# Performance work log

Measured on AMD Instinct MI355X. Metric: run time of the kernel, lower is better.

Reference implementation:

```python
import jax, jax.numpy as jnp
import numpy as np
import math

D_MODEL = 256
H = 8
D_K = D_MODEL // H
POS_OFFSET = 20
GRID = 7  # module hard-codes key_padding_mask.view(bs, 7, 7)


def _sine_pos_table(num_pos_feats=D_MODEL // 2, temperature=10000, rng=(-20, 20)):
    # faithful port of position_embedding_sine with normalize=True
    scale = 2 * math.pi
    emb = np.arange(rng[0], rng[1] + 1, dtype=np.float32)
    emb = emb / (emb[-1] + 1e-6) * scale  # normalize by last element (=20)
    dim_t = np.arange(num_pos_feats, dtype=np.float32)
    dim_t = temperature ** (2.0 * np.floor(dim_t / 2.0) / num_pos_feats)
    pos = emb[:, None] / dim_t  # [41, 128]
    pos = np.stack((np.sin(pos[:, 0::2]), np.cos(pos[:, 1::2])), axis=-1).reshape(pos.shape[0], -1)
    return jnp.asarray(pos, dtype=jnp.float32)  # [41, 128]


def setup_inputs() -> dict:
    key = jax.random.key(0)
    ks = jax.random.split(key, 8)
    L, B, D = 49, 2048, D_MODEL
    query = jax.random.normal(ks[0], (L, B, D), dtype=jnp.float32)
    key_t = jax.random.normal(ks[1], (L, B, D), dtype=jnp.float32)
    value = jax.random.normal(ks[2], (L, B, D), dtype=jnp.float32)
    key_padding_mask = jnp.zeros((B, L), dtype=bool)  # no padding
    # parameters (xavier-ish init)
    lim = math.sqrt(6.0 / (3 * D + D))
    in_proj_weight = jax.random.uniform(ks[3], (3 * D, D), minval=-lim, maxval=lim, dtype=jnp.float32)
    in_proj_bias = jnp.zeros((3 * D,), dtype=jnp.float32)
    out_w = jax.random.uniform(ks[4], (D, D), minval=-1.0 / math.sqrt(D), maxval=1.0 / math.sqrt(D), dtype=jnp.float32)
    out_b = jnp.zeros((D,), dtype=jnp.float32)
    pos_x = _sine_pos_table()  # [41, 128]
    pos_y = _sine_pos_table()  # [41, 128]
    return {"query": query, "key": key_t, "value": value,
            "key_padding_mask": key_padding_mask,
            "in_proj_weight": in_proj_weight, "in_proj_bias": in_proj_bias,
            "out_w": out_w, "out_b": out_b, "pos_x": pos_x, "pos_y": pos_y}


def reference(query, key, value, key_padding_mask, in_proj_weight, in_proj_bias, out_w, out_b, pos_x, pos_y):
    L, B, D = query.shape
    S = key.shape[0]
    scaling = float(D_K) ** -0.5
    w_q, w_k, w_v = in_proj_weight[:D], in_proj_weight[D:2 * D], in_proj_weight[2 * D:]
    b_q, b_k, b_v = in_proj_bias[:D], in_proj_bias[D:2 * D], in_proj_bias[2 * D:]
    q = (query @ w_q.T + b_q) * scaling          # [L, B, D]
    k = key @ w_k.T + b_k                        # [S, B, D]
    v = value @ w_v.T + b_v                      # [S, B, D]
    # [B, H, L, d_k] etc.
    q4 = q.reshape(L, B, H, D_K).transpose(1, 2, 0, 3)
    k4 = k.reshape(S, B, H, D_K).transpose(1, 2, 0, 3)
    v4 = v.reshape(S, B, H, D_K).transpose(1, 2, 0, 3)
    attn = jnp.einsum('bhld,bhsd->bhls', q4, k4)  # [B, H, L, S]
    # relative position indices from cumsum over the 7x7 grid
    img_mask = (~key_padding_mask).reshape(B, GRID, GRID)
    yy = jnp.cumsum(img_mask.astype(jnp.float32), axis=1).reshape(B, -1)
    xx = jnp.cumsum(img_mask.astype(jnp.float32), axis=2).reshape(B, -1)
    idx_yy = (yy[:, :, None] - yy[:, None, :] + POS_OFFSET).astype(jnp.int32)  # [B, HW, HW]
    idx_xx = (xx[:, :, None] - xx[:, None, :] + POS_OFFSET).astype(jnp.int32)
    # project positional tables through the key weights (faithful slicing)
    k_posy = jnp.einsum('pf,df->pd', pos_y, w_k[:, :D // 2])  # [41, D]
    k_posx = jnp.einsum('pf,df->pd', pos_x, w_k[:, D // 2:])  # [41, D]
    P = k_posy.shape[0]
    k_posy = k_posy.reshape(P, H, D_K)
    k_posx = k_posx.reshape(P, H, D_K)
    posy = jnp.einsum('bhld,phd->bhlp', q4, k_posy)  # [B, H, HW, 41]
    posx = jnp.einsum('bhld,phd->bhlp', q4, k_posx)
    gy = jnp.take_along_axis(posy, jnp.broadcast_to(idx_yy[:, None], posy.shape[:3] + (S,)), axis=-1)
    gx = jnp.take_along_axis(posx, jnp.broadcast_to(idx_xx[:, None], posx.shape[:3] + (S,)), axis=-1)
    attn = attn + gy + gx
    attn = jnp.where(key_padding_mask[:, None, None, :], -jnp.inf, attn)
    attn = jax.nn.softmax(attn, axis=-1)  # dropout skipped (eval mode)
    out = jnp.einsum('bhls,bhsd->bhld', attn, v4)        # [B, H, L, d_k]
    out = out.transpose(2, 0, 1, 3).reshape(L, B, D)     # [L, B, D]
    out = out @ out_w.T + out_b
    return out
```

## Files before the change

kernel.cpp:

```cpp
#include <hip/hip_runtime.h>
#include <hip/hip_bf16.h>

#define L_Q 49
#define D_MODEL 256
#define NHEAD 8
#define DK 32
#define PP 41
#define POS_OFF 20

typedef __attribute__((ext_vector_type(8))) __bf16 bf16x8;
typedef __attribute__((ext_vector_type(4))) float f32x4;
typedef __attribute__((ext_vector_type(8))) unsigned short u16x8;

__device__ __forceinline__ float bf2f(unsigned short u) {
    return __uint_as_float(((unsigned)u) << 16);
}
__device__ __forceinline__ unsigned short f2bf(float f) {
    unsigned u = __float_as_uint(f);
    return (unsigned short)((u + 0x7FFF + ((u >> 16) & 1)) >> 16);
}

__global__ __launch_bounds__(256)
void convert_w(const float* __restrict__ W, const float* __restrict__ out_w,
               float scaling,
               unsigned short* __restrict__ wbf, unsigned short* __restrict__ owbf) {
    int i = blockIdx.x * 256 + threadIdx.x;
    if (i < 49152) {
        int row = i >> 6;
        float sc = (row < 256) ? scaling : 1.0f;
        float4 v = reinterpret_cast<const float4*>(W)[i];
        ushort4 o = { f2bf(v.x * sc), f2bf(v.y * sc), f2bf(v.z * sc), f2bf(v.w * sc) };
        reinterpret_cast<ushort4*>(wbf)[i] = o;
    } else {
        float4 v = reinterpret_cast<const float4*>(out_w)[i - 49152];
        ushort4 o = { f2bf(v.x), f2bf(v.y), f2bf(v.z), f2bf(v.w) };
        reinterpret_cast<ushort4*>(owbf)[i - 49152] = o;
    }
}

__global__ __launch_bounds__(256)
void prep_kpos(const float* __restrict__ pos_y, const float* __restrict__ pos_x,
               const float* __restrict__ W, unsigned short* __restrict__ kpb) {
    int p = blockIdx.x;
    int which = blockIdx.y;
    __shared__ float pr[128];
    int d = threadIdx.x;
    if (d < 128) pr[d] = which ? pos_x[p * 128 + d] : pos_y[p * 128 + d];
    __syncthreads();
    const float* Wk = W + 256 * 256;
    int fOff = which ? 128 : 0;
    float acc = 0.f;
    #pragma unroll 8
    for (int f = 0; f < 128; ++f)
        acc += pr[f] * Wk[(size_t)d * 256 + fOff + f];
    kpb[((size_t)which * PP + p) * 256 + d] = f2bf(acc);
}

__global__ __launch_bounds__(512)
void proj_mfma(const float* __restrict__ Xq, const float* __restrict__ Xk,
               const float* __restrict__ Xv,
               const unsigned short* __restrict__ Wb,
               const float* __restrict__ bias, float scaling,
               unsigned short* __restrict__ outq, unsigned short* __restrict__ outk,
               unsigned short* __restrict__ outv) {
    __shared__ unsigned short Wl[65536];
    __shared__ float Lb[256];
    int which = blockIdx.y;
    const float* X = (which == 0) ? Xq : ((which == 1) ? Xk : Xv);
    unsigned short* out = (which == 0) ? outq : ((which == 1) ? outk : outv);
    const unsigned short* wsrc = Wb + (size_t)which * 65536;

    int tid = threadIdx.x, wid = tid >> 6, lane = tid & 63;
    int rgrp = lane & 15, kgrp = lane >> 4;

    #pragma unroll
    for (int it = 0; it < 16; ++it) {
        int c = wid + it * 8;
        unsigned dst = (unsigned)c * 1024 + (unsigned)lane * 16;
        unsigned n = dst >> 9;
        unsigned gs = dst ^ ((n & 7) << 4);
        __builtin_amdgcn_global_load_lds((const char*)wsrc + gs,
                                         (char*)Wl + (size_t)c * 1024, 16, 0, 0);
    }
    if (tid < 256) Lb[tid] = bias[which * 256 + tid] * ((which == 0) ? scaling : 1.0f);

    size_t xrow = (size_t)blockIdx.x * 128 + wid * 16 + rgrp;
    const float* xp = X + xrow * 256 + kgrp * 8;
    float4 pa0 = *reinterpret_cast<const float4*>(xp);
    float4 pa1 = *reinterpret_cast<const float4*>(xp + 4);
    __syncthreads();

    f32x4 acc[16];
    #pragma unroll
    for (int i = 0; i < 16; ++i) acc[i] = (f32x4){0.f, 0.f, 0.f, 0.f};

    unsigned lbase = ((unsigned)rgrp * 512 + (unsigned)kgrp * 16) ^ ((rgrp & 7) << 4);

    #pragma unroll
    for (int kk = 0; kk < 8; ++kk) {
        float4 a0 = pa0, a1 = pa1;
        if (kk < 7) {
            pa0 = *reinterpret_cast<const float4*>(xp + (kk + 1) * 32);
            pa1 = *reinterpret_cast<const float4*>(xp + (kk + 1) * 32 + 4);
        }
        union { unsigned short s[8]; bf16x8 v; } xu;
        xu.s[0] = f2bf(a0.x); xu.s[1] = f2bf(a0.y); xu.s[2] = f2bf(a0.z); xu.s[3] = f2bf(a0.w);
        xu.s[4] = f2bf(a1.x); xu.s[5] = f2bf(a1.y); xu.s[6] = f2bf(a1.z); xu.s[7] = f2bf(a1.w);
        unsigned kb = lbase ^ (unsigned)(kk * 64);
        #pragma unroll
        for (int nt = 0; nt < 16; ++nt) {
            bf16x8 wf = *reinterpret_cast<const bf16x8*>((const char*)Wl + kb + nt * 8192);
            acc[nt] = __builtin_amdgcn_mfma_f32_16x16x32_bf16(wf, xu.v, acc[nt], 0, 0, 0);
        }
    }

    #pragma unroll
    for (int nt = 0; nt < 16; ++nt) {
        float4 bv = *reinterpret_cast<const float4*>(&Lb[nt * 16 + kgrp * 4]);
        ushort4 pk;
        pk.x = f2bf(acc[nt][0] + bv.x);
        pk.y = f2bf(acc[nt][1] + bv.y);
        pk.z = f2bf(acc[nt][2] + bv.z);
        pk.w = f2bf(acc[nt][3] + bv.w);
        *reinterpret_cast<ushort4*>(&out[xrow * 256 + nt * 16 + kgrp * 4]) = pk;
    }
}

__global__ __launch_bounds__(512)
void out_mfma(const unsigned short* __restrict__ Xb, const unsigned short* __restrict__ Wb,
              const float* __restrict__ bias, float* __restrict__ out) {
    __shared__ unsigned short Wl[65536];
    __shared__ float Lb[256];
    int tid = threadIdx.x, wid = tid >> 6, lane = tid & 63;
    int rgrp = lane & 15, kgrp = lane >> 4;

    #pragma unroll
    for (int it = 0; it < 16; ++it) {
        int c = wid + it * 8;
        unsigned dst = (unsigned)c * 1024 + (unsigned)lane * 16;
        unsigned n = dst >> 9;
        unsigned gs = dst ^ ((n & 7) << 4);
        __builtin_amdgcn_global_load_lds((const char*)Wb + gs,
                                         (char*)Wl + (size_t)c * 1024, 16, 0, 0);
    }
    if (tid < 256) Lb[tid] = bias[tid];

    size_t xrow = (size_t)blockIdx.x * 128 + wid * 16 + rgrp;
    const unsigned short* xp = Xb + xrow * 256 + kgrp * 8;
    bf16x8 pa = *reinterpret_cast<const bf16x8*>(xp);
    __syncthreads();

    f32x4 acc[16];
    #pragma unroll
    for (int i = 0; i < 16; ++i) acc[i] = (f32x4){0.f, 0.f, 0.f, 0.f};

    unsigned lbase = ((unsigned)rgrp * 512 + (unsigned)kgrp * 16) ^ ((rgrp & 7) << 4);

    #pragma unroll
    for (int kk = 0; kk < 8; ++kk) {
        bf16x8 af = pa;
        if (kk < 7) pa = *reinterpret_cast<const bf16x8*>(xp + (kk + 1) * 32);
        unsigned kb = lbase ^ (unsigned)(kk * 64);
        #pragma unroll
        for (int nt = 0; nt < 16; ++nt) {
            bf16x8 wf = *reinterpret_cast<const bf16x8*>((const char*)Wl + kb + nt * 8192);
            acc[nt] = __builtin_amdgcn_mfma_f32_16x16x32_bf16(wf, af, acc[nt], 0, 0, 0);
        }
    }

    #pragma unroll
    for (int nt = 0; nt < 16; ++nt) {
        float4 bv = *reinterpret_cast<const float4*>(&Lb[nt * 16 + kgrp * 4]);
        float4 o;
        o.x = acc[nt][0] + bv.x;
        o.y = acc[nt][1] + bv.y;
        o.z = acc[nt][2] + bv.z;
        o.w = acc[nt][3] + bv.w;
        *reinterpret_cast<float4*>(&out[xrow * 256 + nt * 16 + kgrp * 4]) = o;
    }
}

__global__ __launch_bounds__(256)
void attn_mfma(const unsigned short* __restrict__ qbuf,
               const unsigned short* __restrict__ kbuf,
               const unsigned short* __restrict__ vbuf,
               const unsigned short* __restrict__ kpb,
               const unsigned char* __restrict__ mask,
               unsigned short* __restrict__ ctx,
               int B) {
    __shared__ unsigned short Kp[96][40];
    __shared__ unsigned short Pt[64][72];
    __shared__ unsigned short Vt[32][72];
    __shared__ unsigned short postab[49][40];
    __shared__ int yy[L_Q], xx[L_Q];
    __shared__ unsigned char mb[52];

    int b = blockIdx.x, h = blockIdx.y;
    int tid = threadIdx.x, wid = tid >> 6, lane = tid & 63;
    int rgrp = lane & 15, kgrp = lane >> 4;
    size_t lstride = (size_t)B * D_MODEL;
    size_t base = (size_t)b * D_MODEL + (size_t)h * DK;

    if (tid < L_Q) mb[tid] = mask[(size_t)b * L_Q + tid];
    if (tid < 196) {
        int l = tid >> 2, c = tid & 3;
        u16x8 vv = *reinterpret_cast<const u16x8*>(vbuf + (size_t)l * lstride + base + c * 8);
        #pragma unroll
        for (int j = 0; j < 8; ++j) Vt[c * 8 + j][l] = vv[j];
    }
    for (int e = tid; e < 512; e += 256) {
        int d = e >> 4, s2 = 48 + (e & 15);
        if (s2 > 48) Vt[d][s2] = 0;
    }
    for (int t = tid; t < 384; t += 256) {
        int r = t >> 2, kc = t & 3;
        const unsigned short* src;
        if (r < 64) {
            int kr = min(r, 48);
            src = kbuf + (size_t)kr * lstride + base + kc * 8;
        } else if (r < 80) {
            int p = r - 64 + 13;
            src = kpb + (size_t)p * D_MODEL + h * DK + kc * 8;
        } else {
            int p = r - 80 + 13;
            src = kpb + (size_t)(PP + p) * D_MODEL + h * DK + kc * 8;
        }
        *reinterpret_cast<u16x8*>(&Kp[r][kc * 8]) = *reinterpret_cast<const u16x8*>(src);
    }
    __syncthreads();
    if (tid < L_Q) {
        int r = tid / 7, c = tid % 7;
        int sy = 0, sx = 0;
        for (int rr = 0; rr <= r; ++rr) sy += (mb[rr * 7 + c] == 0);
        for (int cc = 0; cc <= c; ++cc) sx += (mb[r * 7 + cc] == 0);
        yy[tid] = sy; xx[tid] = sx;
    }
    __syncthreads();

    int qrow = min(16 * wid + rgrp, 48);
    bf16x8 qfrag = *reinterpret_cast<const bf16x8*>(qbuf + (size_t)qrow * lstride + base + kgrp * 8);
    f32x4 acc[6];
    #pragma unroll
    for (int t = 0; t < 6; ++t) {
        bf16x8 bfrag = *reinterpret_cast<const bf16x8*>(&Kp[t * 16 + rgrp][kgrp * 8]);
        acc[t] = __builtin_amdgcn_mfma_f32_16x16x32_bf16(qfrag, bfrag,
                    (f32x4){0.f, 0.f, 0.f, 0.f}, 0, 0, 0);
    }

    #pragma unroll
    for (int i = 0; i < 4; ++i) {
        int l = 16 * wid + kgrp * 4 + i;
        if (l <= 48) {
            postab[l][rgrp]      = f2bf(acc[4][i]);
            postab[l][20 + rgrp] = f2bf(acc[5][i]);
        }
    }
    asm volatile("s_waitcnt lgkmcnt(0)" ::: "memory");

    #pragma unroll
    for (int i = 0; i < 4; ++i) {
        int l = 16 * wid + kgrp * 4 + i;
        int lc = min(l, 48);
        int yyl = yy[lc], xxl = xx[lc];
        float v[4];
        #pragma unroll
        for (int ct = 0; ct < 4; ++ct) {
            int s = ct * 16 + rgrp;
            int sc = min(s, 48);
            int iy = yyl - yy[sc] + (POS_OFF - 13);
            int ix = xxl - xx[sc] + (POS_OFF - 13);
            float val = acc[ct][i] + bf2f(postab[lc][iy]) + bf2f(postab[lc][20 + ix]);
            v[ct] = (s >= L_Q || mb[sc]) ? -1e30f : val;
        }
        float m = fmaxf(fmaxf(v[0], v[1]), fmaxf(v[2], v[3]));
        m = fmaxf(m, __shfl_xor(m, 1));
        m = fmaxf(m, __shfl_xor(m, 2));
        m = fmaxf(m, __shfl_xor(m, 4));
        m = fmaxf(m, __shfl_xor(m, 8));
        float ssum = 0.f, ex[4];
        #pragma unroll
        for (int ct = 0; ct < 4; ++ct) { ex[ct] = __expf(v[ct] - m); ssum += ex[ct]; }
        ssum += __shfl_xor(ssum, 1);
        ssum += __shfl_xor(ssum, 2);
        ssum += __shfl_xor(ssum, 4);
        ssum += __shfl_xor(ssum, 8);
        float is = 1.f / ssum;
        #pragma unroll
        for (int ct = 0; ct < 4; ++ct)
            Pt[l & 63][ct * 16 + rgrp] = f2bf(ex[ct] * is);
    }
    asm volatile("s_waitcnt lgkmcnt(0)" ::: "memory");

    f32x4 oacc[2];
    oacc[0] = (f32x4){0.f, 0.f, 0.f, 0.f};
    oacc[1] = (f32x4){0.f, 0.f, 0.f, 0.f};
    #pragma unroll
    for (int kc = 0; kc < 2; ++kc) {
        bf16x8 pa = *reinterpret_cast<const bf16x8*>(&Pt[16 * wid + rgrp][kc * 32 + kgrp * 8]);
        #pragma unroll
        for (int dt = 0; dt < 2; ++dt) {
            bf16x8 vb = *reinterpret_cast<const bf16x8*>(&Vt[dt * 16 + rgrp][kc * 32 + kgrp * 8]);
            oacc[dt] = __builtin_amdgcn_mfma_f32_16x16x32_bf16(pa, vb, oacc[dt], 0, 0, 0);
        }
    }
    #pragma unroll
    for (int dt = 0; dt < 2; ++dt)
        #pragma unroll
        for (int i = 0; i < 4; ++i) {
            int l = 16 * wid + kgrp * 4 + i;
            if (l <= 48)
                ctx[(size_t)l * lstride + base + dt * 16 + rgrp] = f2bf(oacc[dt][i]);
        }
}

extern "C" void kernel_launch(void* const* d_in, const int* in_sizes, int n_in,
                              void* d_out, int out_size, void* d_ws, size_t ws_size,
                              hipStream_t stream) {
    const float* query = (const float*)d_in[0];
    const float* key   = (const float*)d_in[1];
    const float* value = (const float*)d_in[2];
    const unsigned char* maskp = (const unsigned char*)d_in[3];
    const float* W     = (const float*)d_in[4];
    const float* bias  = (const float*)d_in[5];
    const float* out_w = (const float*)d_in[6];
    const float* out_b = (const float*)d_in[7];
    const float* pos_x = (const float*)d_in[8];
    const float* pos_y = (const float*)d_in[9];
    float* out = (float*)d_out;

    int B = in_sizes[0] / (L_Q * D_MODEL);
    int M = L_Q * B;

    size_t nqkv = (size_t)M * D_MODEL;
    unsigned short* qb = (unsigned short*)d_ws;
    unsigned short* kb = qb + nqkv;
    unsigned short* vb = kb + nqkv;
    unsigned short* kpb = vb + nqkv;
    unsigned short* wbf = kpb + 2 * PP * D_MODEL;
    unsigned short* owbf = wbf + 768 * 256;

    const float scaling = 0.17677669529663687f;

    convert_w<<<256, 256, 0, stream>>>(W, out_w, scaling, wbf, owbf);
    prep_kpos<<<dim3(PP, 2), 256, 0, stream>>>(pos_y, pos_x, W, kpb);

    int rblocks = M / 128;
    proj_mfma<<<dim3(rblocks, 3), 512, 0, stream>>>(query, key, value, wbf, bias, scaling,
                                                    qb, kb, vb);

    attn_mfma<<<dim3(B, NHEAD), 256, 0, stream>>>(qb, kb, vb, kpb, maskp, qb, B);

    out_mfma<<<rblocks, 512, 0, stream>>>(qb, owbf, out_b, out);
}
```

Baseline: 287.1 us.

## Make projection GEMMs persistent, loading weights once per block with cross-tile prefetch

The QKV projection and output projection kernels become persistent. A fixed grid of 256 blocks per matrix loops over the 784 row tiles, so the 128 KB bf16 weight tile is loaded into LDS once per block instead of once per tile. A 4-deep register ring prefetches the next tile's activations while the current tile's MFMAs run. The fp32-to-bf16 conversion now uses the native __bf16 cast instead of the manual rounding helper. The cost is less parallelism: 256 blocks each use 128 KB of LDS, and the tile count does not divide evenly across blocks, leaving the last wave of tiles unbalanced.

```diff
diff --git a/kernel.cpp b/kernel.cpp
--- a/kernel.cpp
+++ b/kernel.cpp
@@ -62,7 +62,7 @@
                const unsigned short* __restrict__ Wb,
                const float* __restrict__ bias, float scaling,
                unsigned short* __restrict__ outq, unsigned short* __restrict__ outk,
-               unsigned short* __restrict__ outv) {
+               unsigned short* __restrict__ outv, int ntiles) {
     __shared__ unsigned short Wl[65536];
     __shared__ float Lb[256];
     int which = blockIdx.y;
@@ -84,51 +84,62 @@
     }
     if (tid < 256) Lb[tid] = bias[which * 256 + tid] * ((which == 0) ? scaling : 1.0f);
 
-    size_t xrow = (size_t)blockIdx.x * 128 + wid * 16 + rgrp;
-    const float* xp = X + xrow * 256 + kgrp * 8;
-    float4 pa0 = *reinterpret_cast<const float4*>(xp);
-    float4 pa1 = *reinterpret_cast<const float4*>(xp + 4);
-    __syncthreads();
-
-    f32x4 acc[16];
-    #pragma unroll
-    for (int i = 0; i < 16; ++i) acc[i] = (f32x4){0.f, 0.f, 0.f, 0.f};
+    int rowoff = wid * 16 + rgrp;
+    const float* xp = X + ((size_t)blockIdx.x * 128 + rowoff) * 256 + kgrp * 8;
+    float4 ring[4][2];
+    #pragma unroll
+    for (int j = 0; j < 4; ++j) {
+        ring[j][0] = *reinterpret_cast<const float4*>(xp + j * 32);
+        ring[j][1] = *reinterpret_cast<const float4*>(xp + j * 32 + 4);
+    }
+    __syncthreads();
 
     unsigned lbase = ((unsigned)rgrp * 512 + (unsigned)kgrp * 16) ^ ((rgrp & 7) << 4);
 
-    #pragma unroll
-    for (int kk = 0; kk < 8; ++kk) {
-        float4 a0 = pa0, a1 = pa1;
-        if (kk < 7) {
-            pa0 = *reinterpret_cast<const float4*>(xp + (kk + 1) * 32);
-            pa1 = *reinterpret_cast<const float4*>(xp + (kk + 1) * 32 + 4);
-        }
-        union { unsigned short s[8]; bf16x8 v; } xu;
-        xu.s[0] = f2bf(a0.x); xu.s[1] = f2bf(a0.y); xu.s[2] = f2bf(a0.z); xu.s[3] = f2bf(a0.w);
-        xu.s[4] = f2bf(a1.x); xu.s[5] = f2bf(a1.y); xu.s[6] = f2bf(a1.z); xu.s[7] = f2bf(a1.w);
-        unsigned kb = lbase ^ (unsigned)(kk * 64);
+    for (int t = blockIdx.x; t < ntiles; t += 256) {
+        int tn = t + 256;
+        const float* xpn = X + ((size_t)(tn < ntiles ? tn : t) * 128 + rowoff) * 256 + kgrp * 8;
+
+        f32x4 acc[16];
+        #pragma unroll
+        for (int i = 0; i < 16; ++i) acc[i] = (f32x4){0.f, 0.f, 0.f, 0.f};
+
+        #pragma unroll
+        for (int kk = 0; kk < 8; ++kk) {
+            float4 a0 = ring[kk & 3][0];
+            float4 a1 = ring[kk & 3][1];
+            const float* pf = (kk < 4) ? (xp + (kk + 4) * 32) : (xpn + (kk - 4) * 32);
+            ring[kk & 3][0] = *reinterpret_cast<const float4*>(pf);
+            ring[kk & 3][1] = *reinterpret_cast<const float4*>(pf + 4);
+            bf16x8 xv;
+            xv[0] = (__bf16)a0.x; xv[1] = (__bf16)a0.y; xv[2] = (__bf16)a0.z; xv[3] = (__bf16)a0.w;
+            xv[4] = (__bf16)a1.x; xv[5] = (__bf16)a1.y; xv[6] = (__bf16)a1.z; xv[7] = (__bf16)a1.w;
+            unsigned kb = lbase ^ (unsigned)(kk * 64);
+            #pragma unroll
+            for (int nt = 0; nt < 16; ++nt) {
+                bf16x8 wf = *reinterpret_cast<const bf16x8*>((const char*)Wl + kb + nt * 8192);
+                acc[nt] = __builtin_amdgcn_mfma_f32_16x16x32_bf16(wf, xv, acc[nt], 0, 0, 0);
+            }
+        }
+
+        size_t xrow = (size_t)t * 128 + rowoff;
         #pragma unroll
         for (int nt = 0; nt < 16; ++nt) {
-            bf16x8 wf = *reinterpret_cast<const bf16x8*>((const char*)Wl + kb + nt * 8192);
-            acc[nt] = __builtin_amdgcn_mfma_f32_16x16x32_bf16(wf, xu.v, acc[nt], 0, 0, 0);
-        }
-    }
-
-    #pragma unroll
-    for (int nt = 0; nt < 16; ++nt) {
-        float4 bv = *reinterpret_cast<const float4*>(&Lb[nt * 16 + kgrp * 4]);
-        ushort4 pk;
-        pk.x = f2bf(acc[nt][0] + bv.x);
-        pk.y = f2bf(acc[nt][1] + bv.y);
-        pk.z = f2bf(acc[nt][2] + bv.z);
-        pk.w = f2bf(acc[nt][3] + bv.w);
-        *reinterpret_cast<ushort4*>(&out[xrow * 256 + nt * 16 + kgrp * 4]) = pk;
+            float4 bv = *reinterpret_cast<const float4*>(&Lb[nt * 16 + kgrp * 4]);
+            ushort4 pk;
+            pk.x = f2bf(acc[nt][0] + bv.x);
+            pk.y = f2bf(acc[nt][1] + bv.y);
+            pk.z = f2bf(acc[nt][2] + bv.z);
+            pk.w = f2bf(acc[nt][3] + bv.w);
+            *reinterpret_cast<ushort4*>(&out[xrow * 256 + nt * 16 + kgrp * 4]) = pk;
+        }
+        xp = xpn;
     }
 }
 
 __global__ __launch_bounds__(512)
 void out_mfma(const unsigned short* __restrict__ Xb, const unsigned short* __restrict__ Wb,
-              const float* __restrict__ bias, float* __restrict__ out) {
+              const float* __restrict__ bias, float* __restrict__ out, int ntiles) {
     __shared__ unsigned short Wl[65536];
     __shared__ float Lb[256];
     int tid = threadIdx.x, wid = tid >> 6, lane = tid & 63;
@@ -145,38 +156,49 @@
     }
     if (tid < 256) Lb[tid] = bias[tid];
 
-    size_t xrow = (size_t)blockIdx.x * 128 + wid * 16 + rgrp;
-    const unsigned short* xp = Xb + xrow * 256 + kgrp * 8;
-    bf16x8 pa = *reinterpret_cast<const bf16x8*>(xp);
-    __syncthreads();
-
-    f32x4 acc[16];
-    #pragma unroll
-    for (int i = 0; i < 16; ++i) acc[i] = (f32x4){0.f, 0.f, 0.f, 0.f};
+    int rowoff = wid * 16 + rgrp;
+    const unsigned short* xp = Xb + ((size_t)blockIdx.x * 128 + rowoff) * 256 + kgrp * 8;
+    bf16x8 ring[4];
+    #pragma unroll
+    for (int j = 0; j < 4; ++j)
+        ring[j] = *reinterpret_cast<const bf16x8*>(xp + j * 32);
+    __syncthreads();
 
     unsigned lbase = ((unsigned)rgrp * 512 + (unsigned)kgrp * 16) ^ ((rgrp & 7) << 4);
 
-    #pragma unroll
-    for (int kk = 0; kk < 8; ++kk) {
-        bf16x8 af = pa;
-        if (kk < 7) pa = *reinterpret_cast<const bf16x8*>(xp + (kk + 1) * 32);
-        unsigned kb = lbase ^ (unsigned)(kk * 64);
+    for (int t = blockIdx.x; t < ntiles; t += 256) {
+        int tn = t + 256;
+        const unsigned short* xpn = Xb + ((size_t)(tn < ntiles ? tn : t) * 128 + rowoff) * 256 + kgrp * 8;
+
+        f32x4 acc[16];
+        #pragma unroll
+        for (int i = 0; i < 16; ++i) acc[i] = (f32x4){0.f, 0.f, 0.f, 0.f};
+
+        #pragma unroll
+        for (int kk = 0; kk < 8; ++kk) {
+            bf16x8 af = ring[kk & 3];
+            const unsigned short* pf = (kk < 4) ? (xp + (kk + 4) * 32) : (xpn + (kk - 4) * 32);
+            ring[kk & 3] = *reinterpret_cast<const bf16x8*>(pf);
+            unsigned kb = lbase ^ (unsigned)(kk * 64);
+            #pragma unroll
+            for (int nt = 0; nt < 16; ++nt) {
+                bf16x8 wf = *reinterpret_cast<const bf16x8*>((const char*)Wl + kb + nt * 8192);
+                acc[nt] = __builtin_amdgcn_mfma_f32_16x16x32_bf16(wf, af, acc[nt], 0, 0, 0);
+            }
+        }
+
+        size_t xrow = (size_t)t * 128 + rowoff;
         #pragma unroll
         for (int nt = 0; nt < 16; ++nt) {
-            bf16x8 wf = *reinterpret_cast<const bf16x8*>((const char*)Wl + kb + nt * 8192);
-            acc[nt] = __builtin_amdgcn_mfma_f32_16x16x32_bf16(wf, af, acc[nt], 0, 0, 0);
-        }
-    }
-
-    #pragma unroll
-    for (int nt = 0; nt < 16; ++nt) {
-        float4 bv = *reinterpret_cast<const float4*>(&Lb[nt * 16 + kgrp * 4]);
-        float4 o;
-        o.x = acc[nt][0] + bv.x;
-        o.y = acc[nt][1] + bv.y;
-        o.z = acc[nt][2] + bv.z;
-        o.w = acc[nt][3] + bv.w;
-        *reinterpret_cast<float4*>(&out[xrow * 256 + nt * 16 + kgrp * 4]) = o;
+            float4 bv = *reinterpret_cast<const float4*>(&Lb[nt * 16 + kgrp * 4]);
+            float4 o;
+            o.x = acc[nt][0] + bv.x;
+            o.y = acc[nt][1] + bv.y;
+            o.z = acc[nt][2] + bv.z;
+            o.w = acc[nt][3] + bv.w;
+            *reinterpret_cast<float4*>(&out[xrow * 256 + nt * 16 + kgrp * 4]) = o;
+        }
+        xp = xpn;
     }
 }
 
@@ -344,11 +366,11 @@
     convert_w<<<256, 256, 0, stream>>>(W, out_w, scaling, wbf, owbf);
     prep_kpos<<<dim3(PP, 2), 256, 0, stream>>>(pos_y, pos_x, W, kpb);
 
-    int rblocks = M / 128;
-    proj_mfma<<<dim3(rblocks, 3), 512, 0, stream>>>(query, key, value, wbf, bias, scaling,
-                                                    qb, kb, vb);
+    int ntiles = M / 128;
+    proj_mfma<<<dim3(256, 3), 512, 0, stream>>>(query, key, value, wbf, bias, scaling,
+                                                qb, kb, vb, ntiles);
 
     attn_mfma<<<dim3(B, NHEAD), 256, 0, stream>>>(qb, kb, vb, kpb, maskp, qb, B);
 
-    out_mfma<<<rblocks, 512, 0, stream>>>(qb, owbf, out_b, out);
-}
+    out_mfma<<<256, 512, 0, stream>>>(qb, owbf, out_b, out, ntiles);
+}
```

After: 1.093 ms. 281% more time.

## Split projection GEMM tiles across output-column halves to halve LDS per block

Applied to the files above, without the earlier changes.

Both the QKV projection and output projection kernels now compute only half of the 256 output columns per block, loading half the weight matrix into LDS (64 KB instead of 128 KB) and launching twice as many blocks. This is meant to allow more blocks resident per CU and reduce register pressure from the accumulator array, improving occupancy and latency hiding. The cost is that each input row tile is read twice from global memory (fp32 inputs for QKV). The manual bf16 rounding of X is also replaced by native __bf16 conversion.

```diff
diff --git a/kernel.cpp b/kernel.cpp
--- a/kernel.cpp
+++ b/kernel.cpp
@@ -63,18 +63,19 @@
                const float* __restrict__ bias, float scaling,
                unsigned short* __restrict__ outq, unsigned short* __restrict__ outk,
                unsigned short* __restrict__ outv) {
-    __shared__ unsigned short Wl[65536];
-    __shared__ float Lb[256];
+    __shared__ unsigned short Wl[32768];
+    __shared__ float Lb[128];
     int which = blockIdx.y;
+    int t = blockIdx.x >> 1, nhalf = blockIdx.x & 1;
     const float* X = (which == 0) ? Xq : ((which == 1) ? Xk : Xv);
     unsigned short* out = (which == 0) ? outq : ((which == 1) ? outk : outv);
-    const unsigned short* wsrc = Wb + (size_t)which * 65536;
+    const unsigned short* wsrc = Wb + (size_t)which * 65536 + (size_t)nhalf * 32768;
 
     int tid = threadIdx.x, wid = tid >> 6, lane = tid & 63;
     int rgrp = lane & 15, kgrp = lane >> 4;
 
     #pragma unroll
-    for (int it = 0; it < 16; ++it) {
+    for (int it = 0; it < 8; ++it) {
         int c = wid + it * 8;
         unsigned dst = (unsigned)c * 1024 + (unsigned)lane * 16;
         unsigned n = dst >> 9;
@@ -82,17 +83,17 @@
         __builtin_amdgcn_global_load_lds((const char*)wsrc + gs,
                                          (char*)Wl + (size_t)c * 1024, 16, 0, 0);
     }
-    if (tid < 256) Lb[tid] = bias[which * 256 + tid] * ((which == 0) ? scaling : 1.0f);
-
-    size_t xrow = (size_t)blockIdx.x * 128 + wid * 16 + rgrp;
+    if (tid < 128) Lb[tid] = bias[which * 256 + nhalf * 128 + tid] * ((which == 0) ? scaling : 1.0f);
+
+    size_t xrow = (size_t)t * 128 + wid * 16 + rgrp;
     const float* xp = X + xrow * 256 + kgrp * 8;
     float4 pa0 = *reinterpret_cast<const float4*>(xp);
     float4 pa1 = *reinterpret_cast<const float4*>(xp + 4);
     __syncthreads();
 
-    f32x4 acc[16];
-    #pragma unroll
-    for (int i = 0; i < 16; ++i) acc[i] = (f32x4){0.f, 0.f, 0.f, 0.f};
+    f32x4 acc[8];
+    #pragma unroll
+    for (int i = 0; i < 8; ++i) acc[i] = (f32x4){0.f, 0.f, 0.f, 0.f};
 
     unsigned lbase = ((unsigned)rgrp * 512 + (unsigned)kgrp * 16) ^ ((rgrp & 7) << 4);
 
@@ -103,56 +104,58 @@
             pa0 = *reinterpret_cast<const float4*>(xp + (kk + 1) * 32);
             pa1 = *reinterpret_cast<const float4*>(xp + (kk + 1) * 32 + 4);
         }
-        union { unsigned short s[8]; bf16x8 v; } xu;
-        xu.s[0] = f2bf(a0.x); xu.s[1] = f2bf(a0.y); xu.s[2] = f2bf(a0.z); xu.s[3] = f2bf(a0.w);
-        xu.s[4] = f2bf(a1.x); xu.s[5] = f2bf(a1.y); xu.s[6] = f2bf(a1.z); xu.s[7] = f2bf(a1.w);
+        bf16x8 xv;
+        xv[0] = (__bf16)a0.x; xv[1] = (__bf16)a0.y; xv[2] = (__bf16)a0.z; xv[3] = (__bf16)a0.w;
+        xv[4] = (__bf16)a1.x; xv[5] = (__bf16)a1.y; xv[6] = (__bf16)a1.z; xv[7] = (__bf16)a1.w;
         unsigned kb = lbase ^ (unsigned)(kk * 64);
         #pragma unroll
-        for (int nt = 0; nt < 16; ++nt) {
+        for (int nt = 0; nt < 8; ++nt) {
             bf16x8 wf = *reinterpret_cast<const bf16x8*>((const char*)Wl + kb + nt * 8192);
-            acc[nt] = __builtin_amdgcn_mfma_f32_16x16x32_bf16(wf, xu.v, acc[nt], 0, 0, 0);
-        }
-    }
-
-    #pragma unroll
-    for (int nt = 0; nt < 16; ++nt) {
+            acc[nt] = __builtin_amdgcn_mfma_f32_16x16x32_bf16(wf, xv, acc[nt], 0, 0, 0);
+        }
+    }
+
+    #pragma unroll
+    for (int nt = 0; nt < 8; ++nt) {
         float4 bv = *reinterpret_cast<const float4*>(&Lb[nt * 16 + kgrp * 4]);
         ushort4 pk;
         pk.x = f2bf(acc[nt][0] + bv.x);
         pk.y = f2bf(acc[nt][1] + bv.y);
         pk.z = f2bf(acc[nt][2] + bv.z);
         pk.w = f2bf(acc[nt][3] + bv.w);
-        *reinterpret_cast<ushort4*>(&out[xrow * 256 + nt * 16 + kgrp * 4]) = pk;
+        *reinterpret_cast<ushort4*>(&out[xrow * 256 + nhalf * 128 + nt * 16 + kgrp * 4]) = pk;
     }
 }
 
 __global__ __launch_bounds__(512)
 void out_mfma(const unsigned short* __restrict__ Xb, const unsigned short* __restrict__ Wb,
               const float* __restrict__ bias, float* __restrict__ out) {
-    __shared__ unsigned short Wl[65536];
-    __shared__ float Lb[256];
+    __shared__ unsigned short Wl[32768];
+    __shared__ float Lb[128];
+    int t = blockIdx.x >> 1, nhalf = blockIdx.x & 1;
+    const unsigned short* wsrc = Wb + (size_t)nhalf * 32768;
     int tid = threadIdx.x, wid = tid >> 6, lane = tid & 63;
     int rgrp = lane & 15, kgrp = lane >> 4;
 
     #pragma unroll
-    for (int it = 0; it < 16; ++it) {
+    for (int it = 0; it < 8; ++it) {
         int c = wid + it * 8;
         unsigned dst = (unsigned)c * 1024 + (unsigned)lane * 16;
         unsigned n = dst >> 9;
         unsigned gs = dst ^ ((n & 7) << 4);
-        __builtin_amdgcn_global_load_lds((const char*)Wb + gs,
+        __builtin_amdgcn_global_load_lds((const char*)wsrc + gs,
                                          (char*)Wl + (size_t)c * 1024, 16, 0, 0);
     }
-    if (tid < 256) Lb[tid] = bias[tid];
-
-    size_t xrow = (size_t)blockIdx.x * 128 + wid * 16 + rgrp;
+    if (tid < 128) Lb[tid] = bias[nhalf * 128 + tid];
+
+    size_t xrow = (size_t)t * 128 + wid * 16 + rgrp;
     const unsigned short* xp = Xb + xrow * 256 + kgrp * 8;
     bf16x8 pa = *reinterpret_cast<const bf16x8*>(xp);
     __syncthreads();
 
-    f32x4 acc[16];
-    #pragma unroll
-    for (int i = 0; i < 16; ++i) acc[i] = (f32x4){0.f, 0.f, 0.f, 0.f};
+    f32x4 acc[8];
+    #pragma unroll
+    for (int i = 0; i < 8; ++i) acc[i] = (f32x4){0.f, 0.f, 0.f, 0.f};
 
     unsigned lbase = ((unsigned)rgrp * 512 + (unsigned)kgrp * 16) ^ ((rgrp & 7) << 4);
 
@@ -162,21 +165,21 @@
         if (kk < 7) pa = *reinterpret_cast<const bf16x8*>(xp + (kk + 1) * 32);
         unsigned kb = lbase ^ (unsigned)(kk * 64);
         #pragma unroll
-        for (int nt = 0; nt < 16; ++nt) {
+        for (int nt = 0; nt < 8; ++nt) {
             bf16x8 wf = *reinterpret_cast<const bf16x8*>((const char*)Wl + kb + nt * 8192);
             acc[nt] = __builtin_amdgcn_mfma_f32_16x16x32_bf16(wf, af, acc[nt], 0, 0, 0);
         }
     }
 
     #pragma unroll
-    for (int nt = 0; nt < 16; ++nt) {
+    for (int nt = 0; nt < 8; ++nt) {
         float4 bv = *reinterpret_cast<const float4*>(&Lb[nt * 16 + kgrp * 4]);
         float4 o;
         o.x = acc[nt][0] + bv.x;
         o.y = acc[nt][1] + bv.y;
         o.z = acc[nt][2] + bv.z;
         o.w = acc[nt][3] + bv.w;
-        *reinterpret_cast<float4*>(&out[xrow * 256 + nt * 16 + kgrp * 4]) = o;
+        *reinterpret_cast<float4*>(&out[xrow * 256 + nhalf * 128 + nt * 16 + kgrp * 4]) = o;
     }
 }
 
@@ -344,11 +347,11 @@
     convert_w<<<256, 256, 0, stream>>>(W, out_w, scaling, wbf, owbf);
     prep_kpos<<<dim3(PP, 2), 256, 0, stream>>>(pos_y, pos_x, W, kpb);
 
-    int rblocks = M / 128;
-    proj_mfma<<<dim3(rblocks, 3), 512, 0, stream>>>(query, key, value, wbf, bias, scaling,
-                                                    qb, kb, vb);
+    int rblocks2 = (M / 128) * 2;
+    proj_mfma<<<dim3(rblocks2, 3), 512, 0, stream>>>(query, key, value, wbf, bias, scaling,
+                                                     qb, kb, vb);
 
     attn_mfma<<<dim3(B, NHEAD), 256, 0, stream>>>(qb, kb, vb, kpb, maskp, qb, B);
 
-    out_mfma<<<rblocks, 512, 0, stream>>>(qb, owbf, out_b, out);
-}
+    out_mfma<<<rblocks2, 512, 0, stream>>>(qb, owbf, out_b, out);
+}
```

Result: slower. 299.6 us (+4.3%).

## Retile projection GEMMs to 256-row by 64-column blocks with smaller LDS weight slice

Applied to the files above, without the earlier changes.

The QKV and output projection kernels now give each block 256 rows and a quarter of the output columns (64), so only 32 KB of bf16 weights is staged in LDS instead of 128 KB. Each wave computes two 16-row M fragments that share each weight fragment read, which raises MFMA work per LDS read. The smaller LDS footprint should let more blocks fit per CU and cuts per-block weight-load latency. The cost is that each input row is now read four times, once per column-quarter block. The fp32-to-bf16 conversion of inputs also switches from a manual rounding helper to native __bf16 casts.

```diff
diff --git a/kernel.cpp b/kernel.cpp
--- a/kernel.cpp
+++ b/kernel.cpp
@@ -63,120 +63,149 @@
                const float* __restrict__ bias, float scaling,
                unsigned short* __restrict__ outq, unsigned short* __restrict__ outk,
                unsigned short* __restrict__ outv) {
-    __shared__ unsigned short Wl[65536];
-    __shared__ float Lb[256];
+    __shared__ unsigned short Wl[16384];
+    __shared__ float Lb[64];
     int which = blockIdx.y;
+    int t = blockIdx.x >> 2, nq = blockIdx.x & 3;
     const float* X = (which == 0) ? Xq : ((which == 1) ? Xk : Xv);
     unsigned short* out = (which == 0) ? outq : ((which == 1) ? outk : outv);
-    const unsigned short* wsrc = Wb + (size_t)which * 65536;
+    const unsigned short* wsrc = Wb + (size_t)which * 65536 + (size_t)nq * 16384;
 
     int tid = threadIdx.x, wid = tid >> 6, lane = tid & 63;
     int rgrp = lane & 15, kgrp = lane >> 4;
 
     #pragma unroll
-    for (int it = 0; it < 16; ++it) {
+    for (int it = 0; it < 4; ++it) {
         int c = wid + it * 8;
         unsigned dst = (unsigned)c * 1024 + (unsigned)lane * 16;
         unsigned n = dst >> 9;
         unsigned gs = dst ^ ((n & 7) << 4);
         __builtin_amdgcn_global_load_lds((const char*)wsrc + gs,
-                                         (char*)Wl + (size_t)c * 1024, 16, 0, 0);
-    }
-    if (tid < 256) Lb[tid] = bias[which * 256 + tid] * ((which == 0) ? scaling : 1.0f);
-
-    size_t xrow = (size_t)blockIdx.x * 128 + wid * 16 + rgrp;
-    const float* xp = X + xrow * 256 + kgrp * 8;
-    float4 pa0 = *reinterpret_cast<const float4*>(xp);
-    float4 pa1 = *reinterpret_cast<const float4*>(xp + 4);
-    __syncthreads();
-
-    f32x4 acc[16];
-    #pragma unroll
-    for (int i = 0; i < 16; ++i) acc[i] = (f32x4){0.f, 0.f, 0.f, 0.f};
+                                         (char*)Wl + dst, 16, 0, 0);
+    }
+    if (tid < 64) Lb[tid] = bias[which * 256 + nq * 64 + tid] * ((which == 0) ? scaling : 1.0f);
+
+    size_t row0 = (size_t)t * 256 + wid * 32 + rgrp;
+    const float* xp0 = X + row0 * 256 + kgrp * 8;
+    const float* xp1 = xp0 + 16 * 256;
+    float4 pa00 = *reinterpret_cast<const float4*>(xp0);
+    float4 pa01 = *reinterpret_cast<const float4*>(xp0 + 4);
+    float4 pa10 = *reinterpret_cast<const float4*>(xp1);
+    float4 pa11 = *reinterpret_cast<const float4*>(xp1 + 4);
+    __syncthreads();
+
+    f32x4 acc[2][4];
+    #pragma unroll
+    for (int m = 0; m < 2; ++m)
+        #pragma unroll
+        for (int n = 0; n < 4; ++n) acc[m][n] = (f32x4){0.f, 0.f, 0.f, 0.f};
 
     unsigned lbase = ((unsigned)rgrp * 512 + (unsigned)kgrp * 16) ^ ((rgrp & 7) << 4);
 
     #pragma unroll
     for (int kk = 0; kk < 8; ++kk) {
-        float4 a0 = pa0, a1 = pa1;
+        float4 c00 = pa00, c01 = pa01, c10 = pa10, c11 = pa11;
         if (kk < 7) {
-            pa0 = *reinterpret_cast<const float4*>(xp + (kk + 1) * 32);
-            pa1 = *reinterpret_cast<const float4*>(xp + (kk + 1) * 32 + 4);
-        }
-        union { unsigned short s[8]; bf16x8 v; } xu;
-        xu.s[0] = f2bf(a0.x); xu.s[1] = f2bf(a0.y); xu.s[2] = f2bf(a0.z); xu.s[3] = f2bf(a0.w);
-        xu.s[4] = f2bf(a1.x); xu.s[5] = f2bf(a1.y); xu.s[6] = f2bf(a1.z); xu.s[7] = f2bf(a1.w);
+            pa00 = *reinterpret_cast<const float4*>(xp0 + (kk + 1) * 32);
+            pa01 = *reinterpret_cast<const float4*>(xp0 + (kk + 1) * 32 + 4);
+            pa10 = *reinterpret_cast<const float4*>(xp1 + (kk + 1) * 32);
+            pa11 = *reinterpret_cast<const float4*>(xp1 + (kk + 1) * 32 + 4);
+        }
+        bf16x8 x0, x1;
+        x0[0] = (__bf16)c00.x; x0[1] = (__bf16)c00.y; x0[2] = (__bf16)c00.z; x0[3] = (__bf16)c00.w;
+        x0[4] = (__bf16)c01.x; x0[5] = (__bf16)c01.y; x0[6] = (__bf16)c01.z; x0[7] = (__bf16)c01.w;
+        x1[0] = (__bf16)c10.x; x1[1] = (__bf16)c10.y; x1[2] = (__bf16)c10.z; x1[3] = (__bf16)c10.w;
+        x1[4] = (__bf16)c11.x; x1[5] = (__bf16)c11.y; x1[6] = (__bf16)c11.z; x1[7] = (__bf16)c11.w;
         unsigned kb = lbase ^ (unsigned)(kk * 64);
         #pragma unroll
-        for (int nt = 0; nt < 16; ++nt) {
+        for (int nt = 0; nt < 4; ++nt) {
             bf16x8 wf = *reinterpret_cast<const bf16x8*>((const char*)Wl + kb + nt * 8192);
-            acc[nt] = __builtin_amdgcn_mfma_f32_16x16x32_bf16(wf, xu.v, acc[nt], 0, 0, 0);
-        }
-    }
-
-    #pragma unroll
-    for (int nt = 0; nt < 16; ++nt) {
-        float4 bv = *reinterpret_cast<const float4*>(&Lb[nt * 16 + kgrp * 4]);
-        ushort4 pk;
-        pk.x = f2bf(acc[nt][0] + bv.x);
-        pk.y = f2bf(acc[nt][1] + bv.y);
-        pk.z = f2bf(acc[nt][2] + bv.z);
-        pk.w = f2bf(acc[nt][3] + bv.w);
-        *reinterpret_cast<ushort4*>(&out[xrow * 256 + nt * 16 + kgrp * 4]) = pk;
+            acc[0][nt] = __builtin_amdgcn_mfma_f32_16x16x32_bf16(wf, x0, acc[0][nt], 0, 0, 0);
+            acc[1][nt] = __builtin_amdgcn_mfma_f32_16x16x32_bf16(wf, x1, acc[1][nt], 0, 0, 0);
+        }
+    }
+
+    #pragma unroll
+    for (int mf = 0; mf < 2; ++mf) {
+        size_t xrow = row0 + mf * 16;
+        #pragma unroll
+        for (int nt = 0; nt < 4; ++nt) {
+            float4 bv = *reinterpret_cast<const float4*>(&Lb[nt * 16 + kgrp * 4]);
+            ushort4 pk;
+            pk.x = f2bf(acc[mf][nt][0] + bv.x);
+            pk.y = f2bf(acc[mf][nt][1] + bv.y);
+            pk.z = f2bf(acc[mf][nt][2] + bv.z);
+            pk.w = f2bf(acc[mf][nt][3] + bv.w);
+            *reinterpret_cast<ushort4*>(&out[xrow * 256 + nq * 64 + nt * 16 + kgrp * 4]) = pk;
+        }
     }
 }
 
 __global__ __launch_bounds__(512)
 void out_mfma(const unsigned short* __restrict__ Xb, const unsigned short* __restrict__ Wb,
               const float* __restrict__ bias, float* __restrict__ out) {
-    __shared__ unsigned short Wl[65536];
-    __shared__ float Lb[256];
+    __shared__ unsigned short Wl[16384];
+    __shared__ float Lb[64];
+    int t = blockIdx.x >> 2, nq = blockIdx.x & 3;
+    const unsigned short* wsrc = Wb + (size_t)nq * 16384;
     int tid = threadIdx.x, wid = tid >> 6, lane = tid & 63;
     int rgrp = lane & 15, kgrp = lane >> 4;
 
     #pragma unroll
-    for (int it = 0; it < 16; ++it) {
+    for (int it = 0; it < 4; ++it) {
         int c = wid + it * 8;
         unsigned dst = (unsigned)c * 1024 + (unsigned)lane * 16;
         unsigned n = dst >> 9;
         unsigned gs = dst ^ ((n & 7) << 4);
-        __builtin_amdgcn_global_load_lds((const char*)Wb + gs,
-                                         (char*)Wl + (size_t)c * 1024, 16, 0, 0);
-    }
-    if (tid < 256) Lb[tid] = bias[tid];
-
-    size_t xrow = (size_t)blockIdx.x * 128 + wid * 16 + rgrp;
-    const unsigned short* xp = Xb + xrow * 256 + kgrp * 8;
-    bf16x8 pa = *reinterpret_cast<const bf16x8*>(xp);
-    __syncthreads();
-
-    f32x4 acc[16];
-    #pragma unroll
-    for (int i = 0; i < 16; ++i) acc[i] = (f32x4){0.f, 0.f, 0.f, 0.f};
+        __builtin_amdgcn_global_load_lds((const char*)wsrc + gs,
+                                         (char*)Wl + dst, 16, 0, 0);
+    }
+    if (tid < 64) Lb[tid] = bias[nq * 64 + tid];
+
+    size_t row0 = (size_t)t * 256 + wid * 32 + rgrp;
+    const unsigned short* xp0 = Xb + row0 * 256 + kgrp * 8;
+    const unsigned short* xp1 = xp0 + 16 * 256;
+    bf16x8 p0 = *reinterpret_cast<const bf16x8*>(xp0);
+    bf16x8 p1 = *reinterpret_cast<const bf16x8*>(xp1);
+    __syncthreads();
+
+    f32x4 acc[2][4];
+    #pragma unroll
+    for (int m = 0; m < 2; ++m)
+        #pragma unroll
+        for (int n = 0; n < 4; ++n) acc[m][n] = (f32x4){0.f, 0.f, 0.f, 0.f};
 
     unsigned lbase = ((unsigned)rgrp * 512 + (unsigned)kgrp * 16) ^ ((rgrp & 7) << 4);
 
     #pragma unroll
     for (int kk = 0; kk < 8; ++kk) {
-        bf16x8 af = pa;
-        if (kk < 7) pa = *reinterpret_cast<const bf16x8*>(xp + (kk + 1) * 32);
+        bf16x8 a0 = p0, a1 = p1;
+        if (kk < 7) {
+            p0 = *reinterpret_cast<const bf16x8*>(xp0 + (kk + 1) * 32);
+            p1 = *reinterpret_cast<const bf16x8*>(xp1 + (kk + 1) * 32);
+        }
         unsigned kb = lbase ^ (unsigned)(kk * 64);
         #pragma unroll
-        for (int nt = 0; nt < 16; ++nt) {
+        for (int nt = 0; nt < 4; ++nt) {
             bf16x8 wf = *reinterpret_cast<const bf16x8*>((const char*)Wl + kb + nt * 8192);
-            acc[nt] = __builtin_amdgcn_mfma_f32_16x16x32_bf16(wf, af, acc[nt], 0, 0, 0);
-        }
-    }
-
-    #pragma unroll
-    for (int nt = 0; nt < 16; ++nt) {
-        float4 bv = *reinterpret_cast<const float4*>(&Lb[nt * 16 + kgrp * 4]);
-        float4 o;
-        o.x = acc[nt][0] + bv.x;
-        o.y = acc[nt][1] + bv.y;
-        o.z = acc[nt][2] + bv.z;
-        o.w = acc[nt][3] + bv.w;
-        *reinterpret_cast<float4*>(&out[xrow * 256 + nt * 16 + kgrp * 4]) = o;
+            acc[0][nt] = __builtin_amdgcn_mfma_f32_16x16x32_bf16(wf, a0, acc[0][nt], 0, 0, 0);
+            acc[1][nt] = __builtin_amdgcn_mfma_f32_16x16x32_bf16(wf, a1, acc[1][nt], 0, 0, 0);
+        }
+    }
+
+    #pragma unroll
+    for (int mf = 0; mf < 2; ++mf) {
+        size_t xrow = row0 + mf * 16;
+        #pragma unroll
+        for (int nt = 0; nt < 4; ++nt) {
+            float4 bv = *reinterpret_cast<const float4*>(&Lb[nt * 16 + kgrp * 4]);
+            float4 o;
+            o.x = acc[mf][nt][0] + bv.x;
+            o.y = acc[mf][nt][1] + bv.y;
+            o.z = acc[mf][nt][2] + bv.z;
+            o.w = acc[mf][nt][3] + bv.w;
+            *reinterpret_cast<float4*>(&out[xrow * 256 + nq * 64 + nt * 16 + kgrp * 4]) = o;
+        }
     }
 }
 
@@ -344,11 +373,11 @@
     convert_w<<<256, 256, 0, stream>>>(W, out_w, scaling, wbf, owbf);
     prep_kpos<<<dim3(PP, 2), 256, 0, stream>>>(pos_y, pos_x, W, kpb);
 
-    int rblocks = M / 128;
-    proj_mfma<<<dim3(rblocks, 3), 512, 0, stream>>>(query, key, value, wbf, bias, scaling,
+    int gblocks = (M / 256) * 4;
+    proj_mfma<<<dim3(gblocks, 3), 512, 0, stream>>>(query, key, value, wbf, bias, scaling,
                                                     qb, kb, vb);
 
     attn_mfma<<<dim3(B, NHEAD), 256, 0, stream>>>(qb, kb, vb, kpb, maskp, qb, B);
 
-    out_mfma<<<rblocks, 512, 0, stream>>>(qb, owbf, out_b, out);
-}
+    out_mfma<<<gblocks, 512, 0, stream>>>(qb, owbf, out_b, out);
+}
```

Measured after the change: 384.8 us. 34.0% more time.
